# Kernel optimization log

Measured on AMD Instinct MI355X. Metric: run time of the kernel, lower is better.

## Reference

```python
import jax, jax.numpy as jnp
import numpy as np

N, E = 50000, 800000
F_IN, H, OUT = 128, 128, 64
BN_EPS = 1e-5


def gcn_conv(x, W, b, src, dst, n):
    """PyG GCNConv: linear, add self-loops, sym-normalized scatter-add, bias."""
    h = x @ W                                   # [N, H]
    loop = jnp.arange(n)
    s = jnp.concatenate([src, loop])            # [E+N] sources (with self loops)
    d = jnp.concatenate([dst, loop])            # [E+N] destinations
    deg = jax.ops.segment_sum(jnp.ones_like(d, dtype=h.dtype), d, num_segments=n)
    dinv = jnp.where(deg > 0, jax.lax.rsqrt(deg), 0.0)
    norm = dinv[s] * dinv[d]                    # [E+N] D^-1/2 A D^-1/2 weights
    out = jax.ops.segment_sum(h[s] * norm[:, None], d, num_segments=n)
    return out + b


def batchnorm(x, g, b):
    m = x.mean(axis=0)
    v = x.var(axis=0)                           # biased var, matches torch BN fwd
    return g * (x - m) * jax.lax.rsqrt(v + BN_EPS) + b


def setup_inputs() -> dict:
    key = jax.random.key(0)
    ks = jax.random.split(key, 16)
    sc = 1.0 / np.sqrt(H)
    x = jax.random.normal(ks[0], (N, F_IN), dtype=jnp.float32)
    edge_index = jax.random.randint(ks[1], (2, E), 0, N, dtype=jnp.int64)
    return {
        "x": x,
        "edge_index": edge_index,
        "W1": jax.random.normal(ks[2], (F_IN, H), jnp.float32) * sc,
        "b1": jnp.zeros((H,), jnp.float32),
        "g1": jnp.ones((H,), jnp.float32),
        "be1": jnp.zeros((H,), jnp.float32),
        "W2": jax.random.normal(ks[3], (H, H), jnp.float32) * sc,
        "b2": jnp.zeros((H,), jnp.float32),
        "g2": jnp.ones((H,), jnp.float32),
        "be2": jnp.zeros((H,), jnp.float32),
        "W3": jax.random.normal(ks[4], (H, H), jnp.float32) * sc,
        "b3": jnp.zeros((H,), jnp.float32),
        "Wp": jax.random.normal(ks[5], (H, OUT), jnp.float32) * sc,
        "bp": jnp.zeros((OUT,), jnp.float32),
    }


def reference(x, edge_index, W1, b1, g1, be1, W2, b2, g2, be2, W3, b3, Wp, bp):
    src, dst = edge_index[0], edge_index[1]
    n = x.shape[0]
    # layer 1: conv -> BN -> ReLU  (dropout omitted: eval-mode determinism)
    h1 = jax.nn.relu(batchnorm(gcn_conv(x, W1, b1, src, dst, n), g1, be1))
    # layer 2: conv -> BN -> ReLU
    h2 = jax.nn.relu(batchnorm(gcn_conv(h1, W2, b2, src, dst, n), g2, be2))
    # layer 3: conv only
    h3 = gcn_conv(h2, W3, b3, src, dst, n)
    # JumpingKnowledge 'max': elementwise max over layer outputs
    jk = jnp.maximum(jnp.maximum(h1, h2), h3)
    return jk @ Wp + bp
```

## Files before the change

kernel.cpp:

```cpp
#include <hip/hip_runtime.h>

#define F_IN 128
#define H    128
#define OUT  64
#define BN_EPS 1e-5f
#define BIN_BLOCKS 160
#define HIST_BLOCKS 256
#define WCONV_BLOCKS 28
#define BUF_CAP 64
#define OUT_CAP 10240

typedef __attribute__((ext_vector_type(8))) short bf16x8;
typedef __attribute__((ext_vector_type(4))) float f32x4;
typedef __attribute__((ext_vector_type(4))) unsigned uint32x4;
union FragU { unsigned u[4]; bf16x8 f; };

__device__ inline float bflo(unsigned int v) { return __uint_as_float(v << 16); }
__device__ inline float bfhi(unsigned int v) { return __uint_as_float(v & 0xffff0000u); }
__device__ inline unsigned int pack_bf(float a, float b) {
    unsigned int ua = __float_as_uint(a), ub = __float_as_uint(b);
    ua = (ua + 0x7fffu + ((ua >> 16) & 1u)) >> 16;
    ub = (ub + 0x7fffu + ((ub >> 16) & 1u)) >> 16;
    return ua | (ub << 16);
}
union f16u { unsigned short u; _Float16 f; };
__device__ inline unsigned pack_sw(int s, float w) {
    f16u c; c.f = (_Float16)w;
    return (unsigned)s | ((unsigned)c.u << 16);
}
__device__ inline float unpack_w(unsigned p) {
    f16u c; c.u = (unsigned short)(p >> 16);
    return (float)c.f;
}

__global__ __launch_bounds__(256) void k_histw(const int* __restrict__ dst, int* bhs,
                                               float* sums_all, int e,
                                               const float* __restrict__ W1,
                                               const float* __restrict__ W2,
                                               const float* __restrict__ W3,
                                               const float* __restrict__ Wp,
                                               unsigned* __restrict__ wf) {
    __shared__ int h[128];
    const int t = threadIdx.x;
    if (blockIdx.x < HIST_BLOCKS) {
        if (t < 128) h[t] = 0;
        if (blockIdx.x < 2) sums_all[blockIdx.x * 256 + t] = 0.f;
        __syncthreads();
        for (int i = blockIdx.x * 256 + t; i < e; i += HIST_BLOCKS * 256)
            atomicAdd(&h[dst[i] >> 9], 1);
        __syncthreads();
        if (t < 128) bhs[blockIdx.x * 128 + t] = h[t];
        return;
    }
    int g = (blockIdx.x - HIST_BLOCKS) * 256 + t;
    if (g < 6144) {
        int w = g >> 11;
        int rem = g & 2047;
        int ks = rem >> 9;
        int ct = (rem >> 6) & 7;
        int lane = rem & 63;
        const float* W = (w == 0) ? W1 : (w == 1) ? W2 : W3;
        int col = ct * 16 + (lane & 15);
        int kb = ks * 32 + (lane >> 4) * 8;
        uint4 pk;
        pk.x = pack_bf(W[(kb + 0) * 128 + col], W[(kb + 1) * 128 + col]);
        pk.y = pack_bf(W[(kb + 2) * 128 + col], W[(kb + 3) * 128 + col]);
        pk.z = pack_bf(W[(kb + 4) * 128 + col], W[(kb + 5) * 128 + col]);
        pk.w = pack_bf(W[(kb + 6) * 128 + col], W[(kb + 7) * 128 + col]);
        ((uint4*)(wf + (size_t)w * 8192))[(ks * 8 + ct) * 64 + lane] = pk;
    } else if (g < 7168) {
        int rem = g - 6144;
        int ks = rem >> 8;
        int ct = (rem >> 6) & 3;
        int lane = rem & 63;
        int col = ct * 16 + (lane & 15);
        int kb = ks * 32 + (lane >> 4) * 8;
        uint4 pk;
        pk.x = pack_bf(Wp[(kb + 0) * 64 + col], Wp[(kb + 1) * 64 + col]);
        pk.y = pack_bf(Wp[(kb + 2) * 64 + col], Wp[(kb + 3) * 64 + col]);
        pk.z = pack_bf(Wp[(kb + 4) * 64 + col], Wp[(kb + 5) * 64 + col]);
        pk.w = pack_bf(Wp[(kb + 6) * 64 + col], Wp[(kb + 7) * 64 + col]);
        ((uint4*)(wf + 24576))[(ks * 4 + ct) * 64 + lane] = pk;
    }
}

__global__ __launch_bounds__(256) void k_prep(const int* __restrict__ bhs,
                                              int* bstart, int* astart, int* gtail,
                                              int* rowptr, int nb, int n, int e) {
    __shared__ int part[256];
    __shared__ int bs[128];
    const int t = threadIdx.x;
    const int b = t & 127, half = t >> 7;
    int v = 0;
    for (int s = half * (HIST_BLOCKS / 2); s < (half + 1) * (HIST_BLOCKS / 2); s++)
        v += bhs[s * 128 + b];
    part[t] = v;
    __syncthreads();
    int tot = (t < 128) ? (part[t] + part[t + 128]) : 0;
    if (t < 128) bs[t] = tot;
    __syncthreads();
    for (int off = 1; off < 128; off <<= 1) {
        int x = (t < 128 && t >= off) ? bs[t - off] : 0;
        __syncthreads();
        if (t < 128) bs[t] += x;
        __syncthreads();
    }
    if (t < nb) {
        int excl = bs[t] - tot;
        bstart[t] = excl;
        int a = ((excl + 15) & ~15) + 16 * t;
        astart[t] = a;
        gtail[t] = a;
    }
    if (t == 0) { bstart[nb] = e; rowptr[n] = e; }
}

__global__ __launch_bounds__(256) void k_bin(const int* __restrict__ src, const int* __restrict__ dst,
                                             int* gtail, unsigned* ebuck, int e, int nb) {
    __shared__ unsigned buf[128 * BUF_CAP];
    __shared__ int cnt[128];
    const int t = threadIdx.x;
    if (t < 128) cnt[t] = 0;
    __syncthreads();
    const int per = (e + gridDim.x - 1) / gridDim.x;
    const int lo = blockIdx.x * per;
    const int hi = min(e, lo + per);
    for (int base = lo; base < hi; base += 1024) {
#pragma unroll
        for (int k = 0; k < 4; k++) {
            int i = base + k * 256 + t;
            if (i < hi) {
                int d = dst[i];
                int b = d >> 9;
                unsigned entry = (unsigned)src[i] | ((unsigned)(d & 511) << 16);
                int slot = atomicAdd(&cnt[b], 1);
                if (slot < BUF_CAP) buf[b * BUF_CAP + slot] = entry;
                else {
                    int pos = atomicAdd(&gtail[b], 1);
                    __builtin_nontemporal_store(entry, &ebuck[pos]);
                }
            }
        }
        __syncthreads();
        if (t < nb) {
            int c = cnt[t]; if (c > BUF_CAP) c = BUF_CAP;
            int full = c & ~15;
            if (full > 0) {
                int bp = atomicAdd(&gtail[t], full);
                uint32x4* dst4 = (uint32x4*)&ebuck[bp];
                const uint32x4* src4 = (const uint32x4*)&buf[t * BUF_CAP];
                for (int j4 = 0; j4 < (full >> 2); j4++)
                    __builtin_nontemporal_store(src4[j4], &dst4[j4]);
                int rem = c - full;
                for (int j = 0; j < rem; j++) buf[t * BUF_CAP + j] = buf[t * BUF_CAP + full + j];
                cnt[t] = rem;
            }
        }
        __syncthreads();
    }
    if (t < nb) {
        int c = cnt[t]; if (c > BUF_CAP) c = BUF_CAP;
        if (c > 0) {
            int bp = atomicAdd(&gtail[t], c);
            int q = c >> 2;
            uint32x4* dst4 = (uint32x4*)&ebuck[bp];
            const uint32x4* src4 = (const uint32x4*)&buf[t * BUF_CAP];
            for (int j4 = 0; j4 < q; j4++)
                __builtin_nontemporal_store(src4[j4], &dst4[j4]);
            for (int j = q << 2; j < c; j++)
                __builtin_nontemporal_store(buf[t * BUF_CAP + j], &ebuck[bp + j]);
        }
    }
}

__global__ __launch_bounds__(256) void k_placeA(const unsigned* __restrict__ ebuck,
                                                const int* __restrict__ astart,
                                                const int* __restrict__ gtail,
                                                const int* __restrict__ bstart,
                                                int* rowptr, float* dinv, int* sexc, int n) {
    __shared__ int hist[512];
    __shared__ int scn[512];
    const int b = blockIdx.x, t = threadIdx.x;
    hist[t] = 0; hist[t + 256] = 0;
    __syncthreads();
    const int s0 = astart[b], s1 = gtail[b];
    for (int i = s0 + t; i < s1; i += 256) atomicAdd(&hist[ebuck[i] >> 16], 1);
    __syncthreads();
    scn[t] = hist[t]; scn[t + 256] = hist[t + 256];
    __syncthreads();
    for (int off = 1; off < 512; off <<= 1) {
        int a = (t >= off) ? scn[t - off] : 0;
        int c = (t + 256 >= off) ? scn[t + 256 - off] : 0;
        __syncthreads();
        scn[t] += a; scn[t + 256] += c;
        __syncthreads();
    }
    const int nodebase = b << 9;
    const int base = bstart[b];
    int e0 = scn[t] - hist[t];
    int e1 = scn[t + 256] - hist[t + 256];
    sexc[b * 512 + t]       = e0;
    sexc[b * 512 + t + 256] = e1;
    int node = nodebase + t;
    if (node < n) { rowptr[node] = base + e0; dinv[node] = rsqrtf((float)(hist[t] + 1)); }
    node = nodebase + 256 + t;
    if (node < n) { rowptr[node] = base + e1; dinv[node] = rsqrtf((float)(hist[t + 256] + 1)); }
}

__global__ __launch_bounds__(256) void k_placeB(const unsigned* __restrict__ ebuck,
                                                const int* __restrict__ astart,
                                                const int* __restrict__ gtail,
                                                const int* __restrict__ bstart,
                                                const int* __restrict__ sexc,
                                                const float* __restrict__ dinv,
                                                unsigned* epack, int n) {
    __shared__ int hist[512];
    __shared__ int scn[512];
    __shared__ float dloc[512];
    __shared__ unsigned outb[OUT_CAP];
    const int b = blockIdx.x, t = threadIdx.x;
    const int nodebase = b << 9;
    hist[t] = 0; hist[t + 256] = 0;
    scn[t]       = sexc[b * 512 + t];
    scn[t + 256] = sexc[b * 512 + t + 256];
    dloc[t]       = (nodebase + t       < n) ? dinv[nodebase + t]       : 0.f;
    dloc[t + 256] = (nodebase + 256 + t < n) ? dinv[nodebase + 256 + t] : 0.f;
    __syncthreads();
    const int s0 = astart[b], s1 = gtail[b];
    const int base = bstart[b];
    for (int i = s0 + t; i < s1; i += 256) {
        unsigned en = ebuck[i];
        int dlow = en >> 16;
        int s = en & 0xffffu;
        int pos = scn[dlow] + atomicAdd(&hist[dlow], 1);
        unsigned word = pack_sw(s, dinv[s] * dloc[dlow]);
        if (pos < OUT_CAP) outb[pos] = word;
        else __builtin_nontemporal_store(word, &epack[base + pos]);
    }
    __syncthreads();
    int total = s1 - s0; if (total > OUT_CAP) total = OUT_CAP;
    for (int j = t; j < total; j += 256) epack[base + j] = outb[j];
}

__device__ inline void bn_to_lds(const float* __restrict__ sums, const float* __restrict__ g,
                                 const float* __restrict__ be, float* sc_s, float* sh_s,
                                 float inv_n, int tid) {
    if (tid < 128) {
        float m  = sums[tid] * inv_n;
        float v  = sums[128 + tid] * inv_n - m * m;
        float rs = rsqrtf(v + BN_EPS);
        float s  = g[tid] * rs;
        sc_s[tid] = s;
        sh_s[tid] = be[tid] - m * s;
    }
}

template<int MODE>
__global__ __launch_bounds__(256) void k_mm_mfma(const void* __restrict__ Aptr,
                                                 const unsigned* __restrict__ wfrag,
                                                 const float* __restrict__ sums,
                                                 const float* __restrict__ g,
                                                 const float* __restrict__ be, float inv_n,
                                                 unsigned* __restrict__ outb, int n) {
    __shared__ float sc_s[128], sh_s[128];
    __shared__ float dtile[4][16][130];
    const int tid = threadIdx.x;
    if (MODE == 1) {
        bn_to_lds(sums, g, be, sc_s, sh_s, inv_n, tid);
        __syncthreads();
    }
    const int wave = tid >> 6, lane = tid & 63;
    const int r0 = blockIdx.x * 64 + wave * 16;
    const int arow = r0 + (lane & 15);
    const int koff = (lane >> 4) * 8;

    FragU afr[4];
    if (MODE == 0) {
        const float* A = (const float*)Aptr;
#pragma unroll
        for (int ks = 0; ks < 4; ks++) {
            float4 v0 = make_float4(0.f, 0.f, 0.f, 0.f), v1 = v0;
            if (arow < n) {
                v0 = *(const float4*)&A[(size_t)arow * 128 + ks * 32 + koff];
                v1 = *(const float4*)&A[(size_t)arow * 128 + ks * 32 + koff + 4];
            }
            afr[ks].u[0] = pack_bf(v0.x, v0.y);
            afr[ks].u[1] = pack_bf(v0.z, v0.w);
            afr[ks].u[2] = pack_bf(v1.x, v1.y);
            afr[ks].u[3] = pack_bf(v1.z, v1.w);
        }
    } else {
        const unsigned* Ab = (const unsigned*)Aptr;
#pragma unroll
        for (int ks = 0; ks < 4; ks++) {
            uint4 v = make_uint4(0u, 0u, 0u, 0u);
            if (arow < n) v = *(const uint4*)&Ab[(size_t)arow * 64 + ks * 16 + (lane >> 4) * 4];
            unsigned vv[4] = {v.x, v.y, v.z, v.w};
            const int kk = ks * 32 + koff;
#pragma unroll
            for (int q = 0; q < 4; q++) {
                int k0 = kk + 2 * q;
                float lo = fmaxf(fmaf(bflo(vv[q]), sc_s[k0],     sh_s[k0]),     0.f);
                float hi = fmaxf(fmaf(bfhi(vv[q]), sc_s[k0 + 1], sh_s[k0 + 1]), 0.f);
                afr[ks].u[q] = pack_bf(lo, hi);
            }
        }
    }

    const uint4* wf4 = (const uint4*)wfrag;
    const int drow = (lane >> 4) * 4;
#pragma unroll
    for (int ct = 0; ct < 8; ct++) {
        f32x4 acc = {0.f, 0.f, 0.f, 0.f};
#pragma unroll
        for (int ks = 0; ks < 4; ks++) {
            FragU b;
            *(uint4*)b.u = wf4[(ks * 8 + ct) * 64 + lane];
            acc = __builtin_amdgcn_mfma_f32_16x16x32_bf16(afr[ks].f, b.f, acc, 0, 0, 0);
        }
        const int dcol = ct * 16 + (lane & 15);
#pragma unroll
        for (int r = 0; r < 4; r++) dtile[wave][drow + r][dcol] = acc[r];
    }
    const int lr = lane >> 2;
    const int uc = (lane & 3) * 16;
    if (r0 + lr < n) {
#pragma unroll
        for (int q2 = 0; q2 < 4; q2++) {
            const float* s = &dtile[wave][lr][2 * uc + 8 * q2];
            uint4 pk;
            pk.x = pack_bf(s[0], s[1]);
            pk.y = pack_bf(s[2], s[3]);
            pk.z = pack_bf(s[4], s[5]);
            pk.w = pack_bf(s[6], s[7]);
            *(uint4*)&outb[(size_t)(r0 + lr) * 64 + uc + 4 * q2] = pk;
        }
    }
}

__global__ __launch_bounds__(256) void k_jk_mfma(const unsigned* __restrict__ Bb,
                                                 const unsigned* __restrict__ Cb,
                                                 const unsigned* __restrict__ Db,
                                                 const unsigned* __restrict__ wpf,
                                                 const float* __restrict__ sumsL1,
                                                 const float* __restrict__ g1, const float* __restrict__ be1,
                                                 const float* __restrict__ sumsL2,
                                                 const float* __restrict__ g2, const float* __restrict__ be2,
                                                 float inv_n,
                                                 const float* __restrict__ b3,
                                                 const float* __restrict__ bp,
                                                 float* __restrict__ out, int n) {
    __shared__ float sc1[128], sh1[128], sc2[128], sh2[128];
    __shared__ float dtile[4][16][68];
    const int tid = threadIdx.x;
    bn_to_lds(sumsL1, g1, be1, sc1, sh1, inv_n, tid);
    bn_to_lds(sumsL2, g2, be2, sc2, sh2, inv_n, tid);
    __syncthreads();
    const int wave = tid >> 6, lane = tid & 63;
    const int r0 = blockIdx.x * 64 + wave * 16;
    const int arow = r0 + (lane & 15);
    const int koff = (lane >> 4) * 8;

    FragU afr[4];
#pragma unroll
    for (int ks = 0; ks < 4; ks++) {
        uint4 vb = make_uint4(0u,0u,0u,0u), vc = vb, vd = vb;
        if (arow < n) {
            size_t gi = (size_t)arow * 64 + ks * 16 + (lane >> 4) * 4;
            vb = *(const uint4*)&Bb[gi];
            vc = *(const uint4*)&Cb[gi];
            vd = *(const uint4*)&Db[gi];
        }
        unsigned bu[4] = {vb.x, vb.y, vb.z, vb.w};
        unsigned cu[4] = {vc.x, vc.y, vc.z, vc.w};
        unsigned du[4] = {vd.x, vd.y, vd.z, vd.w};
        const int kk = ks * 32 + koff;
#pragma unroll
        for (int q = 0; q < 4; q++) {
            int k0 = kk + 2 * q;
            float h1a = fmaxf(fmaf(bflo(bu[q]), sc1[k0],     sh1[k0]),     0.f);
            float h1b = fmaxf(fmaf(bfhi(bu[q]), sc1[k0 + 1], sh1[k0 + 1]), 0.f);
            float h2a = fmaxf(fmaf(bflo(cu[q]), sc2[k0],     sh2[k0]),     0.f);
            float h2b = fmaxf(fmaf(bfhi(cu[q]), sc2[k0 + 1], sh2[k0 + 1]), 0.f);
            float h3a = bflo(du[q]) + b3[k0];
            float h3b = bfhi(du[q]) + b3[k0 + 1];
            afr[ks].u[q] = pack_bf(fmaxf(fmaxf(h1a, h2a), h3a),
                                   fmaxf(fmaxf(h1b, h2b), h3b));
        }
    }

    const uint4* wf4 = (const uint4*)wpf;
    const int drow = (lane >> 4) * 4;
#pragma unroll
    for (int ct = 0; ct < 4; ct++) {
        f32x4 acc = {0.f, 0.f, 0.f, 0.f};
#pragma unroll
        for (int ks = 0; ks < 4; ks++) {
            FragU b;
            *(uint4*)b.u = wf4[(ks * 4 + ct) * 64 + lane];
            acc = __builtin_amdgcn_mfma_f32_16x16x32_bf16(afr[ks].f, b.f, acc, 0, 0, 0);
        }
        const int dcol = ct * 16 + (lane & 15);
        const float bb = bp[dcol];
#pragma unroll
        for (int r = 0; r < 4; r++) dtile[wave][drow + r][dcol] = acc[r] + bb;
    }
    const int lr = lane >> 2;
    const int uc = (lane & 3) * 16;
    if (r0 + lr < n) {
#pragma unroll
        for (int q2 = 0; q2 < 4; q2++) {
            *(float4*)&out[(size_t)(r0 + lr) * 64 + uc + 4 * q2] =
                *(const float4*)&dtile[wave][lr][uc + 4 * q2];
        }
    }
}

__global__ __launch_bounds__(256) void k_gather_bf(const unsigned int* __restrict__ linb,
                                                   const float* __restrict__ dinv,
                                                   const int* __restrict__ rowptr,
                                                   const unsigned* __restrict__ epack,
                                                   unsigned int* __restrict__ outb, int n) {
    const int t = threadIdx.x & 63;
    int node = blockIdx.x * 4 + (threadIdx.x >> 6);
    if (node >= n) return;
    node = __builtin_amdgcn_readfirstlane(node);
    const float dd = dinv[node];
    int p0 = rowptr[node];
    int p1 = rowptr[node + 1];
    p0 = __builtin_amdgcn_readfirstlane(p0);
    p1 = __builtin_amdgcn_readfirstlane(p1);

    float a0 = 0.f, a1 = 0.f, b0 = 0.f, b1 = 0.f;
    float c0 = 0.f, c1 = 0.f, d0 = 0.f, d1 = 0.f;
    int p = p0;
    for (; p + 16 <= p1; p += 16) {
        unsigned ee[16];
#pragma unroll
        for (int j = 0; j < 16; j++) ee[j] = epack[p + j];
        unsigned vv[16];
#pragma unroll
        for (int j = 0; j < 16; j++) vv[j] = linb[(size_t)(ee[j] & 0xffffu) * 64 + t];
#pragma unroll
        for (int j = 0; j < 16; j += 4) {
            float w0 = unpack_w(ee[j]), w1 = unpack_w(ee[j+1]);
            float w2 = unpack_w(ee[j+2]), w3 = unpack_w(ee[j+3]);
            a0 += bflo(vv[j])   * w0; a1 += bfhi(vv[j])   * w0;
            b0 += bflo(vv[j+1]) * w1; b1 += bfhi(vv[j+1]) * w1;
            c0 += bflo(vv[j+2]) * w2; c1 += bfhi(vv[j+2]) * w2;
            d0 += bflo(vv[j+3]) * w3; d1 += bfhi(vv[j+3]) * w3;
        }
    }
    for (; p + 8 <= p1; p += 8) {
        unsigned e0 = epack[p+0], e1 = epack[p+1], e2 = epack[p+2], e3 = epack[p+3];
        unsigned e4 = epack[p+4], e5 = epack[p+5], e6 = epack[p+6], e7 = epack[p+7];
        unsigned v0 = linb[(size_t)(e0 & 0xffffu) * 64 + t];
        unsigned v1 = linb[(size_t)(e1 & 0xffffu) * 64 + t];
        unsigned v2 = linb[(size_t)(e2 & 0xffffu) * 64 + t];
        unsigned v3 = linb[(size_t)(e3 & 0xffffu) * 64 + t];
        unsigned v4 = linb[(size_t)(e4 & 0xffffu) * 64 + t];
        unsigned v5 = linb[(size_t)(e5 & 0xffffu) * 64 + t];
        unsigned v6 = linb[(size_t)(e6 & 0xffffu) * 64 + t];
        unsigned v7 = linb[(size_t)(e7 & 0xffffu) * 64 + t];
        float w0 = unpack_w(e0), w1 = unpack_w(e1), w2 = unpack_w(e2), w3 = unpack_w(e3);
        float w4 = unpack_w(e4), w5 = unpack_w(e5), w6 = unpack_w(e6), w7 = unpack_w(e7);
        a0 += bflo(v0) * w0; a1 += bfhi(v0) * w0;
        b0 += bflo(v1) * w1; b1 += bfhi(v1) * w1;
        c0 += bflo(v2) * w2; c1 += bfhi(v2) * w2;
        d0 += bflo(v3) * w3; d1 += bfhi(v3) * w3;
        a0 += bflo(v4) * w4; a1 += bfhi(v4) * w4;
        b0 += bflo(v5) * w5; b1 += bfhi(v5) * w5;
        c0 += bflo(v6) * w6; c1 += bfhi(v6) * w6;
        d0 += bflo(v7) * w7; d1 += bfhi(v7) * w7;
    }
    for (; p < p1; p++) {
        unsigned ep = epack[p];
        unsigned v = linb[(size_t)(ep & 0xffffu) * 64 + t];
        float w = unpack_w(ep);
        a0 += bflo(v) * w; a1 += bfhi(v) * w;
    }
    {
        unsigned vs = linb[(size_t)node * 64 + t];
        float wsl = dd * dd;
        a0 += bflo(vs) * wsl; a1 += bfhi(vs) * wsl;
    }
    float F0 = (a0 + b0) + (c0 + d0);
    float F1 = (a1 + b1) + (c1 + d1);
    outb[(size_t)node * 64 + t] = pack_bf(F0, F1);
}

__global__ __launch_bounds__(256) void k_colstats_bf(const unsigned int* __restrict__ hb,
                                                     float* sums, int n) {
    __shared__ float red[4][4][64];
    int t = threadIdx.x & 63, sub = threadIdx.x >> 6;
    int r1 = min(blockIdx.x * 256 + 256, n);
    float s0 = 0.f, s1 = 0.f, q0 = 0.f, q1 = 0.f;
    for (int r = blockIdx.x * 256 + sub; r < r1; r += 4) {
        unsigned int v = hb[(size_t)r * 64 + t];
        float a = bflo(v), b = bfhi(v);
        s0 += a; q0 += a * a;
        s1 += b; q1 += b * b;
    }
    red[0][sub][t] = s0; red[1][sub][t] = s1;
    red[2][sub][t] = q0; red[3][sub][t] = q1;
    __syncthreads();
    if (sub == 0) {
        float ts0 = red[0][0][t] + red[0][1][t] + red[0][2][t] + red[0][3][t];
        float ts1 = red[1][0][t] + red[1][1][t] + red[1][2][t] + red[1][3][t];
        float tq0 = red[2][0][t] + red[2][1][t] + red[2][2][t] + red[2][3][t];
        float tq1 = red[3][0][t] + red[3][1][t] + red[3][2][t] + red[3][3][t];
        atomicAdd(&sums[2 * t],           ts0);
        atomicAdd(&sums[2 * t + 1],       ts1);
        atomicAdd(&sums[128 + 2 * t],     tq0);
        atomicAdd(&sums[128 + 2 * t + 1], tq1);
    }
}

extern "C" void kernel_launch(void* const* d_in, const int* in_sizes, int n_in,
                              void* d_out, int out_size, void* d_ws, size_t ws_size,
                              hipStream_t stream) {
    const float* x   = (const float*)d_in[0];
    const int*   ei  = (const int*)d_in[1];
    const float* W1  = (const float*)d_in[2];
    const float* g1  = (const float*)d_in[4];
    const float* be1 = (const float*)d_in[5];
    const float* W2  = (const float*)d_in[6];
    const float* g2  = (const float*)d_in[8];
    const float* be2 = (const float*)d_in[9];
    const float* W3  = (const float*)d_in[10];
    const float* b3  = (const float*)d_in[11];
    const float* Wp  = (const float*)d_in[12];
    const float* bp  = (const float*)d_in[13];
    float* out = (float*)d_out;

    const int n = in_sizes[0] / F_IN;
    const int e = in_sizes[1] / 2;
    const int* src = ei;
    const int* dst = ei + e;
    const int nb = (n + 511) >> 9;

    float* ws = (float*)d_ws;
    float*        dinv   = ws;
    unsigned int* Ab     = (unsigned int*)(ws + n);
    unsigned int* Bb     = Ab + (size_t)n * 64;
    unsigned int* Cb     = Bb + (size_t)n * 64;
    unsigned int* Db     = Cb + (size_t)n * 64;
    int*          rowptr = (int*)(Db + (size_t)n * 64);
    int*          bstart = rowptr + n + 2;
    int*          astart = bstart + nb + 1;
    int*          gtail  = astart + nb + 1;
    unsigned*     epack  = (unsigned*)(gtail + nb);
    unsigned*     ebuck  = epack + e;
    int*          bhs    = (int*)(ebuck + e + 16 * (nb + 1));
    int*          sexc   = bhs + HIST_BLOCKS * 128;
    float*        sumsL1 = (float*)(sexc + nb * 512);
    float*        sumsL2 = sumsL1 + 256;
    unsigned*     wfr    = (unsigned*)(sumsL2 + 256);

    const int BT = 256;
    const int gN  = (n + BT - 1) / BT;
    const int gMM = (n + 63) / 64;
    const int gG  = (n + 3) / 4;
    const float inv_n = 1.0f / (float)n;

    k_histw<<<HIST_BLOCKS + WCONV_BLOCKS, 256, 0, stream>>>(dst, bhs, sumsL1, e,
                                                            W1, W2, W3, Wp, wfr);
    k_prep<<<1, 256, 0, stream>>>(bhs, bstart, astart, gtail, rowptr, nb, n, e);
    k_bin<<<BIN_BLOCKS, 256, 0, stream>>>(src, dst, gtail, ebuck, e, nb);
    k_placeA<<<nb, 256, 0, stream>>>(ebuck, astart, gtail, bstart, rowptr, dinv, sexc, n);
    k_placeB<<<nb, 256, 0, stream>>>(ebuck, astart, gtail, bstart, sexc, dinv, epack, n);

    k_mm_mfma<0><<<gMM, 256, 0, stream>>>(x, wfr, nullptr, nullptr, nullptr, 0.f, Ab, n);
    k_gather_bf<<<gG, 256, 0, stream>>>(Ab, dinv, rowptr, epack, Bb, n);
    k_colstats_bf<<<gN, 256, 0, stream>>>(Bb, sumsL1, n);

    k_mm_mfma<1><<<gMM, 256, 0, stream>>>(Bb, wfr + 8192, sumsL1, g1, be1, inv_n, Ab, n);
    k_gather_bf<<<gG, 256, 0, stream>>>(Ab, dinv, rowptr, epack, Cb, n);
    k_colstats_bf<<<gN, 256, 0, stream>>>(Cb, sumsL2, n);

    k_mm_mfma<1><<<gMM, 256, 0, stream>>>(Cb, wfr + 16384, sumsL2, g2, be2, inv_n, Ab, n);
    k_gather_bf<<<gG, 256, 0, stream>>>(Ab, dinv, rowptr, epack, Db, n);

    k_jk_mfma<<<gMM, 256, 0, stream>>>(Bb, Cb, Db, wfr + 24576,
                                       sumsL1, g1, be1, sumsL2, g2, be2,
                                       inv_n, b3, bp, out, n);
}
```

Measured before the change: 315.1 us.

## Fuse BatchNorm column statistics into gather kernel with sharded atomic accumulators

Removes the separate column-statistics kernel by having each gather block reduce the sums and sums of squares of its four freshly written rows and atomically add them into one of 32 shadow accumulator copies. The BN consumers then add up the 32 shadows. This saves one launch and one full re-read of the 50000x128 bf16 activations per layer. The cost is a __syncthreads and atomics in every 4-node block, about 12500 blocks each issuing 256 atomics spread over 32 shadows, which could cause atomic contention.

```diff
diff --git a/kernel.cpp b/kernel.cpp
--- a/kernel.cpp
+++ b/kernel.cpp
@@ -7,6 +7,7 @@
 #define BIN_BLOCKS 160
 #define HIST_BLOCKS 256
 #define WCONV_BLOCKS 28
+#define NSHADOW 32
 #define BUF_CAP 64
 #define OUT_CAP 10240
 
@@ -44,7 +45,8 @@
     const int t = threadIdx.x;
     if (blockIdx.x < HIST_BLOCKS) {
         if (t < 128) h[t] = 0;
-        if (blockIdx.x < 2) sums_all[blockIdx.x * 256 + t] = 0.f;
+        if (blockIdx.x < 2 * NSHADOW)
+            sums_all[blockIdx.x * 256 + t] = 0.f;
         __syncthreads();
         for (int i = blockIdx.x * 256 + t; i < e; i += HIST_BLOCKS * 256)
             atomicAdd(&h[dst[i] >> 9], 1);
@@ -246,12 +248,18 @@
                                  const float* __restrict__ be, float* sc_s, float* sh_s,
                                  float inv_n, int tid) {
     if (tid < 128) {
-        float m  = sums[tid] * inv_n;
-        float v  = sums[128 + tid] * inv_n - m * m;
+        float s = 0.f, q = 0.f;
+#pragma unroll
+        for (int c = 0; c < NSHADOW; c++) {
+            s += sums[c * 256 + tid];
+            q += sums[c * 256 + 128 + tid];
+        }
+        float m  = s * inv_n;
+        float v  = q * inv_n - m * m;
         float rs = rsqrtf(v + BN_EPS);
-        float s  = g[tid] * rs;
-        sc_s[tid] = s;
-        sh_s[tid] = be[tid] - m * s;
+        float sf = g[tid] * rs;
+        sc_s[tid] = sf;
+        sh_s[tid] = be[tid] - m * sf;
     }
 }
 
@@ -416,103 +424,98 @@
     }
 }
 
+template<int STATS>
 __global__ __launch_bounds__(256) void k_gather_bf(const unsigned int* __restrict__ linb,
                                                    const float* __restrict__ dinv,
                                                    const int* __restrict__ rowptr,
                                                    const unsigned* __restrict__ epack,
-                                                   unsigned int* __restrict__ outb, int n) {
+                                                   unsigned int* __restrict__ outb,
+                                                   float* __restrict__ sums, int n) {
+    __shared__ float red[4][4][64];
     const int t = threadIdx.x & 63;
-    int node = blockIdx.x * 4 + (threadIdx.x >> 6);
-    if (node >= n) return;
-    node = __builtin_amdgcn_readfirstlane(node);
-    const float dd = dinv[node];
-    int p0 = rowptr[node];
-    int p1 = rowptr[node + 1];
-    p0 = __builtin_amdgcn_readfirstlane(p0);
-    p1 = __builtin_amdgcn_readfirstlane(p1);
-
-    float a0 = 0.f, a1 = 0.f, b0 = 0.f, b1 = 0.f;
-    float c0 = 0.f, c1 = 0.f, d0 = 0.f, d1 = 0.f;
-    int p = p0;
-    for (; p + 16 <= p1; p += 16) {
-        unsigned ee[16];
-#pragma unroll
-        for (int j = 0; j < 16; j++) ee[j] = epack[p + j];
-        unsigned vv[16];
-#pragma unroll
-        for (int j = 0; j < 16; j++) vv[j] = linb[(size_t)(ee[j] & 0xffffu) * 64 + t];
-#pragma unroll
-        for (int j = 0; j < 16; j += 4) {
-            float w0 = unpack_w(ee[j]), w1 = unpack_w(ee[j+1]);
-            float w2 = unpack_w(ee[j+2]), w3 = unpack_w(ee[j+3]);
-            a0 += bflo(vv[j])   * w0; a1 += bfhi(vv[j])   * w0;
-            b0 += bflo(vv[j+1]) * w1; b1 += bfhi(vv[j+1]) * w1;
-            c0 += bflo(vv[j+2]) * w2; c1 += bfhi(vv[j+2]) * w2;
-            d0 += bflo(vv[j+3]) * w3; d1 += bfhi(vv[j+3]) * w3;
-        }
-    }
-    for (; p + 8 <= p1; p += 8) {
-        unsigned e0 = epack[p+0], e1 = epack[p+1], e2 = epack[p+2], e3 = epack[p+3];
-        unsigned e4 = epack[p+4], e5 = epack[p+5], e6 = epack[p+6], e7 = epack[p+7];
-        unsigned v0 = linb[(size_t)(e0 & 0xffffu) * 64 + t];
-        unsigned v1 = linb[(size_t)(e1 & 0xffffu) * 64 + t];
-        unsigned v2 = linb[(size_t)(e2 & 0xffffu) * 64 + t];
-        unsigned v3 = linb[(size_t)(e3 & 0xffffu) * 64 + t];
-        unsigned v4 = linb[(size_t)(e4 & 0xffffu) * 64 + t];
-        unsigned v5 = linb[(size_t)(e5 & 0xffffu) * 64 + t];
-        unsigned v6 = linb[(size_t)(e6 & 0xffffu) * 64 + t];
-        unsigned v7 = linb[(size_t)(e7 & 0xffffu) * 64 + t];
-        float w0 = unpack_w(e0), w1 = unpack_w(e1), w2 = unpack_w(e2), w3 = unpack_w(e3);
-        float w4 = unpack_w(e4), w5 = unpack_w(e5), w6 = unpack_w(e6), w7 = unpack_w(e7);
-        a0 += bflo(v0) * w0; a1 += bfhi(v0) * w0;
-        b0 += bflo(v1) * w1; b1 += bfhi(v1) * w1;
-        c0 += bflo(v2) * w2; c1 += bfhi(v2) * w2;
-        d0 += bflo(v3) * w3; d1 += bfhi(v3) * w3;
-        a0 += bflo(v4) * w4; a1 += bfhi(v4) * w4;
-        b0 += bflo(v5) * w5; b1 += bfhi(v5) * w5;
-        c0 += bflo(v6) * w6; c1 += bfhi(v6) * w6;
-        d0 += bflo(v7) * w7; d1 += bfhi(v7) * w7;
-    }
-    for (; p < p1; p++) {
-        unsigned ep = epack[p];
-        unsigned v = linb[(size_t)(ep & 0xffffu) * 64 + t];
-        float w = unpack_w(ep);
-        a0 += bflo(v) * w; a1 += bfhi(v) * w;
-    }
-    {
-        unsigned vs = linb[(size_t)node * 64 + t];
-        float wsl = dd * dd;
-        a0 += bflo(vs) * wsl; a1 += bfhi(vs) * wsl;
-    }
-    float F0 = (a0 + b0) + (c0 + d0);
-    float F1 = (a1 + b1) + (c1 + d1);
-    outb[(size_t)node * 64 + t] = pack_bf(F0, F1);
-}
-
-__global__ __launch_bounds__(256) void k_colstats_bf(const unsigned int* __restrict__ hb,
-                                                     float* sums, int n) {
-    __shared__ float red[4][4][64];
-    int t = threadIdx.x & 63, sub = threadIdx.x >> 6;
-    int r1 = min(blockIdx.x * 256 + 256, n);
-    float s0 = 0.f, s1 = 0.f, q0 = 0.f, q1 = 0.f;
-    for (int r = blockIdx.x * 256 + sub; r < r1; r += 4) {
-        unsigned int v = hb[(size_t)r * 64 + t];
-        float a = bflo(v), b = bfhi(v);
-        s0 += a; q0 += a * a;
-        s1 += b; q1 += b * b;
-    }
-    red[0][sub][t] = s0; red[1][sub][t] = s1;
-    red[2][sub][t] = q0; red[3][sub][t] = q1;
-    __syncthreads();
-    if (sub == 0) {
-        float ts0 = red[0][0][t] + red[0][1][t] + red[0][2][t] + red[0][3][t];
-        float ts1 = red[1][0][t] + red[1][1][t] + red[1][2][t] + red[1][3][t];
-        float tq0 = red[2][0][t] + red[2][1][t] + red[2][2][t] + red[2][3][t];
-        float tq1 = red[3][0][t] + red[3][1][t] + red[3][2][t] + red[3][3][t];
-        atomicAdd(&sums[2 * t],           ts0);
-        atomicAdd(&sums[2 * t + 1],       ts1);
-        atomicAdd(&sums[128 + 2 * t],     tq0);
-        atomicAdd(&sums[128 + 2 * t + 1], tq1);
+    const int wave = threadIdx.x >> 6;
+    int node = blockIdx.x * 4 + wave;
+    float F0 = 0.f, F1 = 0.f;
+    if (node < n) {
+        node = __builtin_amdgcn_readfirstlane(node);
+        const float dd = dinv[node];
+        int p0 = __builtin_amdgcn_readfirstlane(rowptr[node]);
+        int p1 = __builtin_amdgcn_readfirstlane(rowptr[node + 1]);
+
+        float a0 = 0.f, a1 = 0.f, b0 = 0.f, b1 = 0.f;
+        float c0 = 0.f, c1 = 0.f, d0 = 0.f, d1 = 0.f;
+        int p = p0;
+        for (; p + 16 <= p1; p += 16) {
+            unsigned ee[16];
+#pragma unroll
+            for (int j = 0; j < 16; j++) ee[j] = epack[p + j];
+            unsigned vv[16];
+#pragma unroll
+            for (int j = 0; j < 16; j++) vv[j] = linb[(size_t)(ee[j] & 0xffffu) * 64 + t];
+#pragma unroll
+            for (int j = 0; j < 16; j += 4) {
+                float w0 = unpack_w(ee[j]), w1 = unpack_w(ee[j+1]);
+                float w2 = unpack_w(ee[j+2]), w3 = unpack_w(ee[j+3]);
+                a0 += bflo(vv[j])   * w0; a1 += bfhi(vv[j])   * w0;
+                b0 += bflo(vv[j+1]) * w1; b1 += bfhi(vv[j+1]) * w1;
+                c0 += bflo(vv[j+2]) * w2; c1 += bfhi(vv[j+2]) * w2;
+                d0 += bflo(vv[j+3]) * w3; d1 += bfhi(vv[j+3]) * w3;
+            }
+        }
+        for (; p + 8 <= p1; p += 8) {
+            unsigned e0 = epack[p+0], e1 = epack[p+1], e2 = epack[p+2], e3 = epack[p+3];
+            unsigned e4 = epack[p+4], e5 = epack[p+5], e6 = epack[p+6], e7 = epack[p+7];
+            unsigned v0 = linb[(size_t)(e0 & 0xffffu) * 64 + t];
+            unsigned v1 = linb[(size_t)(e1 & 0xffffu) * 64 + t];
+            unsigned v2 = linb[(size_t)(e2 & 0xffffu) * 64 + t];
+            unsigned v3 = linb[(size_t)(e3 & 0xffffu) * 64 + t];
+            unsigned v4 = linb[(size_t)(e4 & 0xffffu) * 64 + t];
+            unsigned v5 = linb[(size_t)(e5 & 0xffffu) * 64 + t];
+            unsigned v6 = linb[(size_t)(e6 & 0xffffu) * 64 + t];
+            unsigned v7 = linb[(size_t)(e7 & 0xffffu) * 64 + t];
+            float w0 = unpack_w(e0), w1 = unpack_w(e1), w2 = unpack_w(e2), w3 = unpack_w(e3);
+            float w4 = unpack_w(e4), w5 = unpack_w(e5), w6 = unpack_w(e6), w7 = unpack_w(e7);
+            a0 += bflo(v0) * w0; a1 += bfhi(v0) * w0;
+            b0 += bflo(v1) * w1; b1 += bfhi(v1) * w1;
+            c0 += bflo(v2) * w2; c1 += bfhi(v2) * w2;
+            d0 += bflo(v3) * w3; d1 += bfhi(v3) * w3;
+            a0 += bflo(v4) * w4; a1 += bfhi(v4) * w4;
+            b0 += bflo(v5) * w5; b1 += bfhi(v5) * w5;
+            c0 += bflo(v6) * w6; c1 += bfhi(v6) * w6;
+            d0 += bflo(v7) * w7; d1 += bfhi(v7) * w7;
+        }
+        for (; p < p1; p++) {
+            unsigned ep = epack[p];
+            unsigned v = linb[(size_t)(ep & 0xffffu) * 64 + t];
+            float w = unpack_w(ep);
+            a0 += bflo(v) * w; a1 += bfhi(v) * w;
+        }
+        {
+            unsigned vs = linb[(size_t)node * 64 + t];
+            float wsl = dd * dd;
+            a0 += bflo(vs) * wsl; a1 += bfhi(vs) * wsl;
+        }
+        float rx = (a0 + b0) + (c0 + d0);
+        float ry = (a1 + b1) + (c1 + d1);
+        unsigned pk = pack_bf(rx, ry);
+        outb[(size_t)node * 64 + t] = pk;
+        if (STATS) { F0 = bflo(pk); F1 = bfhi(pk); }
+    }
+    if (STATS) {
+        red[0][wave][t] = F0;       red[1][wave][t] = F1;
+        red[2][wave][t] = F0 * F0;  red[3][wave][t] = F1 * F1;
+        __syncthreads();
+        if (threadIdx.x < 64) {
+            float ts0 = red[0][0][t] + red[0][1][t] + red[0][2][t] + red[0][3][t];
+            float ts1 = red[1][0][t] + red[1][1][t] + red[1][2][t] + red[1][3][t];
+            float tq0 = red[2][0][t] + red[2][1][t] + red[2][2][t] + red[2][3][t];
+            float tq1 = red[3][0][t] + red[3][1][t] + red[3][2][t] + red[3][3][t];
+            float* base = sums + (blockIdx.x & (NSHADOW - 1)) * 256;
+            atomicAdd(&base[2 * t],           ts0);
+            atomicAdd(&base[2 * t + 1],       ts1);
+            atomicAdd(&base[128 + 2 * t],     tq0);
+            atomicAdd(&base[128 + 2 * t + 1], tq1);
+        }
     }
 }
 
@@ -554,11 +557,9 @@
     int*          bhs    = (int*)(ebuck + e + 16 * (nb + 1));
     int*          sexc   = bhs + HIST_BLOCKS * 128;
     float*        sumsL1 = (float*)(sexc + nb * 512);
-    float*        sumsL2 = sumsL1 + 256;
-    unsigned*     wfr    = (unsigned*)(sumsL2 + 256);
-
-    const int BT = 256;
-    const int gN  = (n + BT - 1) / BT;
+    float*        sumsL2 = sumsL1 + NSHADOW * 256;
+    unsigned*     wfr    = (unsigned*)(sumsL2 + NSHADOW * 256);
+
     const int gMM = (n + 63) / 64;
     const int gG  = (n + 3) / 4;
     const float inv_n = 1.0f / (float)n;
@@ -571,15 +572,13 @@
     k_placeB<<<nb, 256, 0, stream>>>(ebuck, astart, gtail, bstart, sexc, dinv, epack, n);
 
     k_mm_mfma<0><<<gMM, 256, 0, stream>>>(x, wfr, nullptr, nullptr, nullptr, 0.f, Ab, n);
-    k_gather_bf<<<gG, 256, 0, stream>>>(Ab, dinv, rowptr, epack, Bb, n);
-    k_colstats_bf<<<gN, 256, 0, stream>>>(Bb, sumsL1, n);
+    k_gather_bf<1><<<gG, 256, 0, stream>>>(Ab, dinv, rowptr, epack, Bb, sumsL1, n);
 
     k_mm_mfma<1><<<gMM, 256, 0, stream>>>(Bb, wfr + 8192, sumsL1, g1, be1, inv_n, Ab, n);
-    k_gather_bf<<<gG, 256, 0, stream>>>(Ab, dinv, rowptr, epack, Cb, n);
-    k_colstats_bf<<<gN, 256, 0, stream>>>(Cb, sumsL2, n);
+    k_gather_bf<1><<<gG, 256, 0, stream>>>(Ab, dinv, rowptr, epack, Cb, sumsL2, n);
 
     k_mm_mfma<1><<<gMM, 256, 0, stream>>>(Cb, wfr + 16384, sumsL2, g2, be2, inv_n, Ab, n);
-    k_gather_bf<<<gG, 256, 0, stream>>>(Ab, dinv, rowptr, epack, Db, n);
+    k_gather_bf<0><<<gG, 256, 0, stream>>>(Ab, dinv, rowptr, epack, Db, nullptr, n);
 
     k_jk_mfma<<<gMM, 256, 0, stream>>>(Bb, Cb, Db, wfr + 24576,
                                        sumsL1, g1, be1, sumsL2, g2, be2,
```

Result: faster. 297.0 us, median of 2 (-5.7%).
